# Kernel optimization log

Measured on AMD Instinct MI355X. Metric: run time of the kernel, lower is better.

The kernel has to match this reference:

```python
import jax, jax.numpy as jnp
import numpy as np

C = 256
NUM_HEADS = 4
GROUPS = 8
EPS = 1e-5


def setup_inputs() -> dict:
    key = jax.random.key(0)
    ks = jax.random.split(key, 7)
    B, H, W = 4, 64, 64
    x = jax.random.normal(ks[0], (B, C, H, W), dtype=jnp.float32)
    # GroupNorm affine params
    norm_w = jnp.ones((C,), dtype=jnp.float32)
    norm_b = jnp.zeros((C,), dtype=jnp.float32)
    # 1x1 convs == channel-mixing matrices
    qkv_w = jax.random.normal(ks[1], (3 * C, C), dtype=jnp.float32) * (C ** -0.5)
    qkv_b = jnp.zeros((3 * C,), dtype=jnp.float32)
    proj_w = jax.random.normal(ks[2], (C, C), dtype=jnp.float32) * (C ** -0.5)
    proj_b = jnp.zeros((C,), dtype=jnp.float32)
    return {"x": x, "norm_w": norm_w, "norm_b": norm_b,
            "qkv_w": qkv_w, "qkv_b": qkv_b,
            "proj_w": proj_w, "proj_b": proj_b}


def _group_norm(x, w, b):
    B, Cc, H, W = x.shape
    xr = x.reshape(B, GROUPS, Cc // GROUPS, H * W)
    mean = xr.mean(axis=(2, 3), keepdims=True)
    var = xr.var(axis=(2, 3), keepdims=True)
    xn = ((xr - mean) * jax.lax.rsqrt(var + EPS)).reshape(B, Cc, H, W)
    return xn * w[None, :, None, None] + b[None, :, None, None]


def reference(x, norm_w, norm_b, qkv_w, qkv_b, proj_w, proj_b):
    B, Cc, H, W = x.shape
    nh = NUM_HEADS
    d = Cc // nh
    h = _group_norm(x, norm_w, norm_b)
    # 1x1 conv: channel matmul
    qkv = jnp.einsum('oc,bchw->bohw', qkv_w, h) + qkv_b[None, :, None, None]
    q, k, v = jnp.split(qkv, 3, axis=1)
    q = q.reshape(B, nh, d, H * W)
    k = k.reshape(B, nh, d, H * W)
    v = v.reshape(B, nh, d, H * W)
    scale = d ** -0.5
    attn = jnp.einsum('bhci,bhcj->bhij', q, k) * scale  # [B, nh, HW, HW]
    attn = jax.nn.softmax(attn, axis=-1)
    o = jnp.einsum('bhij,bhcj->bhci', attn, v).reshape(B, Cc, H, W)
    out = jnp.einsum('oc,bchw->bohw', proj_w, o) + proj_b[None, :, None, None]
    return x + out
```

## Files before the change

kernel.cpp:

```cpp
#include <hip/hip_runtime.h>

typedef unsigned short u16;
typedef __attribute__((ext_vector_type(8))) short bf16x8;
typedef __attribute__((ext_vector_type(4))) float f32x4;
typedef __attribute__((ext_vector_type(16))) float f32x16;
typedef __attribute__((ext_vector_type(2))) int i32x2;

#define MFMA16(A, B, C) __builtin_amdgcn_mfma_f32_16x16x32_bf16((A), (B), (C), 0, 0, 0)
#define MFMA32(A, B, C) __builtin_amdgcn_mfma_f32_32x32x16_bf16((A), (B), (C), 0, 0, 0)

#define BB 4
#define CC 256
#define HW 4096
#define NH 4
#define HD 64

#define QSCALE 0.18033688f

__device__ __forceinline__ u16 f2bf(float f) {
  unsigned int u = __builtin_bit_cast(unsigned int, f);
  u += 0x7fffu + ((u >> 16) & 1u);
  return (u16)(u >> 16);
}

__device__ __forceinline__ unsigned cvtpk(float a, float b) {
  unsigned r;
  asm("v_cvt_pk_bf16_f32 %0, %1, %2" : "=v"(r) : "v"(a), "v"(b));
  return r;
}

__global__ __launch_bounds__(256) void w2bf_kernel(const float* __restrict__ qw,
                                                   const float* __restrict__ pw,
                                                   u16* __restrict__ wbf) {
  int idx = (blockIdx.x * 256 + threadIdx.x) * 4;
  const int NQ = 768 * 256;
  const float* src = (idx < NQ) ? (qw + idx) : (pw + (idx - NQ));
  float4 v = *(const float4*)src;
  union { u16 u[4]; uint2 w; } pk;
  pk.u[0] = f2bf(v.x); pk.u[1] = f2bf(v.y);
  pk.u[2] = f2bf(v.z); pk.u[3] = f2bf(v.w);
  *(uint2*)(wbf + idx) = pk.w;
}

__global__ __launch_bounds__(256) void gn_partial_kernel(const float* __restrict__ x,
                                                         float* __restrict__ partial) {
  const float4* p = (const float4*)(x + (size_t)blockIdx.x * 16384);
  float s = 0.f, ss = 0.f;
  for (int i = threadIdx.x; i < 4096; i += 256) {
    float4 v = p[i];
    s += (v.x + v.y) + (v.z + v.w);
    ss += (v.x * v.x + v.y * v.y) + (v.z * v.z + v.w * v.w);
  }
#pragma unroll
  for (int msk = 32; msk; msk >>= 1) {
    s += __shfl_xor(s, msk);
    ss += __shfl_xor(ss, msk);
  }
  __shared__ float red[2][4];
  int wave = threadIdx.x >> 6;
  if ((threadIdx.x & 63) == 0) { red[0][wave] = s; red[1][wave] = ss; }
  __syncthreads();
  if (threadIdx.x == 0) {
    partial[blockIdx.x] = red[0][0] + red[0][1] + red[0][2] + red[0][3];
    partial[256 + blockIdx.x] = red[1][0] + red[1][1] + red[1][2] + red[1][3];
  }
}

__global__ __launch_bounds__(64) void gn_final_kernel(const float* __restrict__ partial,
                                                      float* __restrict__ stats) {
  int bg = threadIdx.x;
  if (bg < 32) {
    float S = 0.f, SS = 0.f;
#pragma unroll
    for (int sp = 0; sp < 8; ++sp) {
      S += partial[bg * 8 + sp];
      SS += partial[256 + bg * 8 + sp];
    }
    const float invN = 1.0f / 131072.0f;
    float mean = S * invN;
    float var = SS * invN - mean * mean;
    stats[bg] = mean;
    stats[32 + bg] = rsqrtf(var + 1e-5f);
  }
}

__global__ __launch_bounds__(256) void norm_t_kernel(const float* __restrict__ x,
                                                     const float* __restrict__ nw,
                                                     const float* __restrict__ nb,
                                                     const float* __restrict__ stats,
                                                     u16* __restrict__ h_t) {
  int b = blockIdx.y;
  int s = blockIdx.x * 64 + (threadIdx.x & 63);
  int w = threadIdx.x >> 6;
  const float* xb = x + (size_t)b * CC * HW;
  u16* hb = h_t + ((size_t)b * HW + s) * CC;
#pragma unroll
  for (int cc = 0; cc < 8; ++cc) {
    int c0 = w * 64 + cc * 8;
    union { u16 u[8]; uint4 v; } pk;
#pragma unroll
    for (int j = 0; j < 8; ++j) {
      int c = c0 + j;
      int g = c >> 5;
      float mean = stats[b * 8 + g];
      float rstd = stats[32 + b * 8 + g];
      float a = nw[c] * rstd;
      float bb2 = nb[c] - mean * a;
      float vv = xb[(size_t)c * HW + s];
      pk.u[j] = f2bf(vv * a + bb2);
    }
    *(uint4*)(hb + c0) = pk.v;
  }
}

__global__ __launch_bounds__(256) void gemm_qk_kernel(const u16* __restrict__ h_t,
                                                      const u16* __restrict__ wbf,
                                                      const float* __restrict__ qb,
                                                      u16* __restrict__ q_t,
                                                      u16* __restrict__ k_f) {
  int b = blockIdx.z;
  int lane = threadIdx.x & 63, wave = threadIdx.x >> 6;
  int lr = lane & 15, lg = lane >> 4;
  int m0 = blockIdx.x * 128 + (wave >> 1) * 64;
  int n0 = blockIdx.y * 128 + (wave & 1) * 64;
  const u16* hb = h_t + (size_t)b * HW * CC;
  f32x4 acc[4][4] = {};
  for (int kc = 0; kc < 8; ++kc) {
    int ko = kc * 32 + lg * 8;
    bf16x8 af[4], bfr[4];
#pragma unroll
    for (int mi = 0; mi < 4; ++mi)
      af[mi] = *(const bf16x8*)(hb + (size_t)(m0 + mi * 16 + lr) * CC + ko);
#pragma unroll
    for (int ni = 0; ni < 4; ++ni)
      bfr[ni] = *(const bf16x8*)(wbf + (size_t)(n0 + ni * 16 + lr) * CC + ko);
#pragma unroll
    for (int mi = 0; mi < 4; ++mi)
#pragma unroll
      for (int ni = 0; ni < 4; ++ni)
        acc[mi][ni] = MFMA16(af[mi], bfr[ni], acc[mi][ni]);
  }
  bool isq = (blockIdx.y < 2);
  if (isq) {
#pragma unroll
    for (int ni = 0; ni < 4; ++ni) {
      int o = n0 + ni * 16 + lr;
      float bias = qb[o];
      u16* dp = q_t + (((size_t)b * NH + (o >> 6)) * HW) * HD + (o & 63);
#pragma unroll
      for (int mi = 0; mi < 4; ++mi)
#pragma unroll
        for (int r = 0; r < 4; ++r) {
          int s = m0 + mi * 16 + lg * 4 + r;
          dp[(size_t)s * HD] = f2bf((acc[mi][ni][r] + bias) * QSCALE);
        }
    }
  } else {
#pragma unroll
    for (int ni = 0; ni < 4; ++ni) {
      int o = n0 + ni * 16 + lr;
      int oc = o - 256;
      int h = oc >> 6, c = oc & 63;
      int kc = c >> 4, hi2 = (c >> 3) & 1, j = c & 7;
      float bias = qb[o];
      u16* base = k_f + (size_t)(b * NH + h) * HW * HD;
#pragma unroll
      for (int mi = 0; mi < 4; ++mi)
#pragma unroll
        for (int r = 0; r < 4; ++r) {
          int s = m0 + mi * 16 + lg * 4 + r;
          int jb32 = s >> 5, ql2 = s & 31;
          base[((size_t)(jb32 * 4 + kc) * 64 + hi2 * 32 + ql2) * 8 + j] =
              f2bf(acc[mi][ni][r] + bias);
        }
    }
  }
}

__global__ __launch_bounds__(256) void gemm_v_kernel(const u16* __restrict__ h_t,
                                                     const u16* __restrict__ wbf,
                                                     const float* __restrict__ qb,
                                                     u16* __restrict__ v_f) {
  int b = blockIdx.z;
  int lane = threadIdx.x & 63, wave = threadIdx.x >> 6;
  int lr = lane & 15, lg = lane >> 4;
  int m0 = blockIdx.y * 128 + (wave >> 1) * 64;
  int n0 = blockIdx.x * 128 + (wave & 1) * 64;
  const u16* hb = h_t + (size_t)b * HW * CC;
  f32x4 acc[4][4] = {};
  for (int kc = 0; kc < 8; ++kc) {
    int ko = kc * 32 + lg * 8;
    bf16x8 af[4], bfr[4];
#pragma unroll
    for (int mi = 0; mi < 4; ++mi)
      af[mi] = *(const bf16x8*)(wbf + (size_t)(512 + m0 + mi * 16 + lr) * CC + ko);
#pragma unroll
    for (int ni = 0; ni < 4; ++ni)
      bfr[ni] = *(const bf16x8*)(hb + (size_t)(n0 + ni * 16 + lr) * CC + ko);
#pragma unroll
    for (int mi = 0; mi < 4; ++mi)
#pragma unroll
      for (int ni = 0; ni < 4; ++ni)
        acc[mi][ni] = MFMA16(af[mi], bfr[ni], acc[mi][ni]);
  }
#pragma unroll
  for (int mi = 0; mi < 4; ++mi)
#pragma unroll
    for (int r = 0; r < 4; ++r) {
      int o = m0 + mi * 16 + lg * 4 + r;
      int h = o >> 6, c = o & 63;
      int half = c >> 5, qlc = c & 31;
      float bias = qb[512 + o];
      u16* base = v_f + (size_t)(b * NH + h) * HW * HD;
#pragma unroll
      for (int ni = 0; ni < 4; ++ni) {
        int s = n0 + ni * 16 + lr;
        int jb64 = s >> 6, w = s & 63;
        int kc = w >> 4, hi2 = (w >> 3) & 1, j = w & 7;
        base[((size_t)((jb64 * 2 + half) * 4 + kc) * 64 + hi2 * 32 + qlc) * 8 + j] =
            f2bf(acc[mi][ni][r] + bias);
      }
    }
}

__global__ __launch_bounds__(256) void attn_kernel(const u16* __restrict__ q_t,
                                                   const u16* __restrict__ k_f,
                                                   const u16* __restrict__ v_f,
                                                   u16* __restrict__ o_t) {
  int bh = blockIdx.y;
  int tid = threadIdx.x;
  int wave = tid >> 6, lane = tid & 63;
  int ql = lane & 31, hi = lane >> 5;
  int q0w = blockIdx.x * 128 + wave * 32;
  const u16* qp = q_t + (size_t)bh * HW * HD;
  const u16* kfb = k_f + (size_t)bh * HW * HD + lane * 8;
  const u16* vfb = v_f + (size_t)bh * HW * HD + lane * 8;

  bf16x8 qf[4];
#pragma unroll
  for (int kc = 0; kc < 4; ++kc)
    qf[kc] = *(const bf16x8*)(qp + (size_t)(q0w + ql) * HD + kc * 16 + hi * 8);

  float l_run = 0.f;
  f32x16 of0 = {}, of1 = {};
  bf16x8 kfr[8], vfr[8];

#pragma unroll
  for (int kc = 0; kc < 4; ++kc) {
    kfr[kc] = *(const bf16x8*)(kfb + (size_t)kc * 512);
    kfr[4 + kc] = *(const bf16x8*)(kfb + (size_t)(4 + kc) * 512);
  }

#pragma unroll 1
  for (int it = 0; it < 64; ++it) {
    const u16* vb = vfb + (size_t)it * 8 * 512;
#pragma unroll
    for (int kc = 0; kc < 4; ++kc) {
      vfr[kc] = *(const bf16x8*)(vb + (size_t)kc * 512);
      vfr[4 + kc] = *(const bf16x8*)(vb + (size_t)(4 + kc) * 512);
    }

    f32x16 s0 = {}, s1 = {};
    __builtin_amdgcn_s_setprio(1);
#pragma unroll
    for (int kc = 0; kc < 4; ++kc) {
      s0 = MFMA32(kfr[kc], qf[kc], s0);
      s1 = MFMA32(kfr[4 + kc], qf[kc], s1);
    }
    __builtin_amdgcn_s_setprio(0);

    if (it < 63) {
      const u16* kb = kfb + (size_t)(it + 1) * 8 * 512;
#pragma unroll
      for (int kc = 0; kc < 4; ++kc) {
        kfr[kc] = *(const bf16x8*)(kb + (size_t)kc * 512);
        kfr[4 + kc] = *(const bf16x8*)(kb + (size_t)(4 + kc) * 512);
      }
    }

#pragma unroll
    for (int i = 0; i < 16; ++i) {
      s0[i] = __builtin_amdgcn_exp2f(s0[i]);
      s1[i] = __builtin_amdgcn_exp2f(s1[i]);
    }

    bf16x8 pf[4];
#pragma unroll
    for (int kc = 0; kc < 4; ++kc) {
      const f32x16 pv = (kc < 2) ? s0 : s1;
      const int b8 = (kc & 1) * 8;
      unsigned A0 = cvtpk(pv[b8 + 0], pv[b8 + 1]);
      unsigned A1 = cvtpk(pv[b8 + 2], pv[b8 + 3]);
      unsigned B0 = cvtpk(pv[b8 + 4], pv[b8 + 5]);
      unsigned B1 = cvtpk(pv[b8 + 6], pv[b8 + 7]);
      i32x2 r0 = __builtin_amdgcn_permlane32_swap((int)A0, (int)B0, false, false);
      i32x2 r1 = __builtin_amdgcn_permlane32_swap((int)A1, (int)B1, false, false);
      union { unsigned w[4]; bf16x8 v8; } u;
      u.w[0] = (unsigned)r0[0]; u.w[1] = (unsigned)r1[0];
      u.w[2] = (unsigned)r0[1]; u.w[3] = (unsigned)r1[1];
      pf[kc] = u.v8;
    }

    __builtin_amdgcn_s_setprio(1);
#pragma unroll
    for (int kc = 0; kc < 4; ++kc) {
      of0 = MFMA32(vfr[kc], pf[kc], of0);
      of1 = MFMA32(vfr[4 + kc], pf[kc], of1);
    }
    __builtin_amdgcn_s_setprio(0);

    float t8[8];
#pragma unroll
    for (int i = 0; i < 8; ++i)
      t8[i] = (s0[i] + s0[i + 8]) + (s1[i] + s1[i + 8]);
    float t4a = t8[0] + t8[4], t4b = t8[1] + t8[5];
    float t4c = t8[2] + t8[6], t4d = t8[3] + t8[7];
    l_run += (t4a + t4b) + (t4c + t4d);
  }

  float l_tot = l_run + __shfl_xor(l_run, 32);
  float inv_l = 1.0f / l_tot;
  int bb = bh >> 2, hh = bh & 3;
  u16* orow = o_t + ((size_t)bb * HW + q0w + ql) * CC + hh * 64;
#pragma unroll
  for (int cb = 0; cb < 2; ++cb) {
    const f32x16 o = cb ? of1 : of0;
#pragma unroll
    for (int t = 0; t < 4; ++t) {
      int c0 = cb * 32 + t * 8 + hi * 4;
      union { u16 u[4]; uint2 w; } pk;
#pragma unroll
      for (int r = 0; r < 4; ++r) pk.u[r] = f2bf(o[t * 4 + r] * inv_l);
      *(uint2*)(orow + c0) = pk.w;
    }
  }
}

__global__ __launch_bounds__(256) void proj_kernel(const u16* __restrict__ o_t,
                                                   const u16* __restrict__ wbf,
                                                   const float* __restrict__ pb,
                                                   const float* __restrict__ x,
                                                   float* __restrict__ out) {
  int b = blockIdx.z;
  int lane = threadIdx.x & 63, wave = threadIdx.x >> 6;
  int lr = lane & 15, lg = lane >> 4;
  int m0 = blockIdx.x * 128 + (wave >> 1) * 64;
  int n0 = blockIdx.y * 128 + (wave & 1) * 64;
  const u16* ob = o_t + (size_t)b * HW * CC;
  const u16* pwbf = wbf + (size_t)768 * CC;
  f32x4 acc[4][4] = {};
  for (int kc = 0; kc < 8; ++kc) {
    int ko = kc * 32 + lg * 8;
    bf16x8 af[4], bfr[4];
#pragma unroll
    for (int mi = 0; mi < 4; ++mi)
      af[mi] = *(const bf16x8*)(ob + (size_t)(m0 + mi * 16 + lr) * CC + ko);
#pragma unroll
    for (int ni = 0; ni < 4; ++ni)
      bfr[ni] = *(const bf16x8*)(pwbf + (size_t)(n0 + ni * 16 + lr) * CC + ko);
#pragma unroll
    for (int mi = 0; mi < 4; ++mi)
#pragma unroll
      for (int ni = 0; ni < 4; ++ni)
        acc[mi][ni] = MFMA16(af[mi], bfr[ni], acc[mi][ni]);
  }
#pragma unroll
  for (int ni = 0; ni < 4; ++ni) {
    int o = n0 + ni * 16 + lr;
    float bias = pb[o];
    const float* xp = x + ((size_t)b * CC + o) * HW;
    float* op = out + ((size_t)b * CC + o) * HW;
#pragma unroll
    for (int mi = 0; mi < 4; ++mi) {
      int sb = m0 + mi * 16 + lg * 4;
      float4 xv = *(const float4*)(xp + sb);
      float4 res;
      res.x = acc[mi][ni][0] + bias + xv.x;
      res.y = acc[mi][ni][1] + bias + xv.y;
      res.z = acc[mi][ni][2] + bias + xv.z;
      res.w = acc[mi][ni][3] + bias + xv.w;
      *(float4*)(op + sb) = res;
    }
  }
}

extern "C" void kernel_launch(void* const* d_in, const int* in_sizes, int n_in,
                              void* d_out, int out_size, void* d_ws, size_t ws_size,
                              hipStream_t stream) {
  const float* x = (const float*)d_in[0];
  const float* nw = (const float*)d_in[1];
  const float* nb = (const float*)d_in[2];
  const float* qw = (const float*)d_in[3];
  const float* qb = (const float*)d_in[4];
  const float* pw = (const float*)d_in[5];
  const float* pb = (const float*)d_in[6];
  float* out = (float*)d_out;

  float* stats = (float*)d_ws;
  float* partial = stats + 64;
  u16* h_t = (u16*)((char*)d_ws + 4096);
  u16* q_t = h_t + (size_t)BB * HW * CC;
  u16* k_f = q_t + (size_t)BB * HW * CC;
  u16* v_f = k_f + (size_t)BB * HW * CC;
  u16* wbf = v_f + (size_t)BB * HW * CC;
  u16* o_t = h_t;

  gn_partial_kernel<<<256, 256, 0, stream>>>(x, partial);
  gn_final_kernel<<<1, 64, 0, stream>>>(partial, stats);
  w2bf_kernel<<<256, 256, 0, stream>>>(qw, pw, wbf);
  norm_t_kernel<<<dim3(HW / 64, BB), 256, 0, stream>>>(x, nw, nb, stats, h_t);
  gemm_qk_kernel<<<dim3(HW / 128, 4, BB), 256, 0, stream>>>(h_t, wbf, qb, q_t, k_f);
  gemm_v_kernel<<<dim3(HW / 128, 2, BB), 256, 0, stream>>>(h_t, wbf, qb, v_f);
  attn_kernel<<<dim3(HW / 128, BB * NH), 256, 0, stream>>>(q_t, k_f, v_f, o_t);
  proj_kernel<<<dim3(HW / 128, 2, BB), 256, 0, stream>>>(o_t, wbf, pb, x, out);
}
```

Measured before the change: 160.3 us.

## Split attention key loop across two wave halves and merge via shared memory

Doubles the attention block to 512 threads. Two groups of four waves each handle alternate key tiles for the same 128 queries. Partial output accumulators and row sums from the second group are reduced through shared memory before normalization and store. This adds more in-flight waves per query tile to hide memory and MFMA latency, and halves each wave's serial loop length. The cost is a shared-memory reduction, extra barriers and higher register and LDS pressure per block. Skipping max-subtraction keeps the split merge exact.

After: 154.0 us. 1.04x faster.

```diff
diff --git a/kernel.cpp b/kernel.cpp
--- a/kernel.cpp
+++ b/kernel.cpp
@@ -223,15 +223,17 @@
     }
 }
 
-__global__ __launch_bounds__(256) void attn_kernel(const u16* __restrict__ q_t,
+__global__ __launch_bounds__(512) void attn_kernel(const u16* __restrict__ q_t,
                                                    const u16* __restrict__ k_f,
                                                    const u16* __restrict__ v_f,
                                                    u16* __restrict__ o_t) {
+  __shared__ float mbuf[4 * 33 * 64];
   int bh = blockIdx.y;
   int tid = threadIdx.x;
   int wave = tid >> 6, lane = tid & 63;
+  int half = wave >> 2, wsub = wave & 3;
   int ql = lane & 31, hi = lane >> 5;
-  int q0w = blockIdx.x * 128 + wave * 32;
+  int q0w = blockIdx.x * 128 + wsub * 32;
   const u16* qp = q_t + (size_t)bh * HW * HD;
   const u16* kfb = k_f + (size_t)bh * HW * HD + lane * 8;
   const u16* vfb = v_f + (size_t)bh * HW * HD + lane * 8;
@@ -245,14 +247,17 @@
   f32x16 of0 = {}, of1 = {};
   bf16x8 kfr[8], vfr[8];
 
-#pragma unroll
-  for (int kc = 0; kc < 4; ++kc) {
-    kfr[kc] = *(const bf16x8*)(kfb + (size_t)kc * 512);
-    kfr[4 + kc] = *(const bf16x8*)(kfb + (size_t)(4 + kc) * 512);
+  {
+    const u16* kb = kfb + (size_t)half * 8 * 512;
+#pragma unroll
+    for (int kc = 0; kc < 4; ++kc) {
+      kfr[kc] = *(const bf16x8*)(kb + (size_t)kc * 512);
+      kfr[4 + kc] = *(const bf16x8*)(kb + (size_t)(4 + kc) * 512);
+    }
   }
 
 #pragma unroll 1
-  for (int it = 0; it < 64; ++it) {
+  for (int it = half; it < 64; it += 2) {
     const u16* vb = vfb + (size_t)it * 8 * 512;
 #pragma unroll
     for (int kc = 0; kc < 4; ++kc) {
@@ -269,8 +274,8 @@
     }
     __builtin_amdgcn_s_setprio(0);
 
-    if (it < 63) {
-      const u16* kb = kfb + (size_t)(it + 1) * 8 * 512;
+    if (it < 62) {
+      const u16* kb = kfb + (size_t)(it + 2) * 8 * 512;
 #pragma unroll
       for (int kc = 0; kc < 4; ++kc) {
         kfr[kc] = *(const bf16x8*)(kb + (size_t)kc * 512);
@@ -318,20 +323,38 @@
     l_run += (t4a + t4b) + (t4c + t4d);
   }
 
-  float l_tot = l_run + __shfl_xor(l_run, 32);
-  float inv_l = 1.0f / l_tot;
-  int bb = bh >> 2, hh = bh & 3;
-  u16* orow = o_t + ((size_t)bb * HW + q0w + ql) * CC + hh * 64;
-#pragma unroll
-  for (int cb = 0; cb < 2; ++cb) {
-    const f32x16 o = cb ? of1 : of0;
-#pragma unroll
-    for (int t = 0; t < 4; ++t) {
-      int c0 = cb * 32 + t * 8 + hi * 4;
-      union { u16 u[4]; uint2 w; } pk;
-#pragma unroll
-      for (int r = 0; r < 4; ++r) pk.u[r] = f2bf(o[t * 4 + r] * inv_l);
-      *(uint2*)(orow + c0) = pk.w;
+  __syncthreads();
+  if (half == 1) {
+    float* mb = mbuf + (size_t)wsub * 33 * 64 + lane;
+#pragma unroll
+    for (int i = 0; i < 16; ++i) mb[i * 64] = of0[i];
+#pragma unroll
+    for (int i = 0; i < 16; ++i) mb[(16 + i) * 64] = of1[i];
+    mb[32 * 64] = l_run;
+  }
+  __syncthreads();
+  if (half == 0) {
+    const float* mb = mbuf + (size_t)wsub * 33 * 64 + lane;
+#pragma unroll
+    for (int i = 0; i < 16; ++i) of0[i] += mb[i * 64];
+#pragma unroll
+    for (int i = 0; i < 16; ++i) of1[i] += mb[(16 + i) * 64];
+    l_run += mb[32 * 64];
+    float l_tot = l_run + __shfl_xor(l_run, 32);
+    float inv_l = 1.0f / l_tot;
+    int bb = bh >> 2, hh = bh & 3;
+    u16* orow = o_t + ((size_t)bb * HW + q0w + ql) * CC + hh * 64;
+#pragma unroll
+    for (int cb = 0; cb < 2; ++cb) {
+      const f32x16 o = cb ? of1 : of0;
+#pragma unroll
+      for (int t = 0; t < 4; ++t) {
+        int c0 = cb * 32 + t * 8 + hi * 4;
+        union { u16 u[4]; uint2 w; } pk;
+#pragma unroll
+        for (int r = 0; r < 4; ++r) pk.u[r] = f2bf(o[t * 4 + r] * inv_l);
+        *(uint2*)(orow + c0) = pk.w;
+      }
     }
   }
 }
@@ -411,6 +434,6 @@
   norm_t_kernel<<<dim3(HW / 64, BB), 256, 0, stream>>>(x, nw, nb, stats, h_t);
   gemm_qk_kernel<<<dim3(HW / 128, 4, BB), 256, 0, stream>>>(h_t, wbf, qb, q_t, k_f);
   gemm_v_kernel<<<dim3(HW / 128, 2, BB), 256, 0, stream>>>(h_t, wbf, qb, v_f);
-  attn_kernel<<<dim3(HW / 128, BB * NH), 256, 0, stream>>>(q_t, k_f, v_f, o_t);
+  attn_kernel<<<dim3(HW / 128, BB * NH), 512, 0, stream>>>(q_t, k_f, v_f, o_t);
   proj_kernel<<<dim3(HW / 128, 2, BB), 256, 0, stream>>>(o_t, wbf, pb, x, out);
 }
```
